# Kernel tuning notes

Hardware: AMD Instinct MI355X
Metric: run time of the kernel (lower is better)

Reference implementation:

```python
import jax, jax.numpy as jnp
import numpy as np

B, L, D, H = 32, 1024, 512, 512
ODE_STEPS = 6
DT = 1.0

def _unif(key, shape, fan_in):
    bound = 1.0 / np.sqrt(fan_in)
    return jax.random.uniform(key, shape, jnp.float32, -bound, bound)

def setup_inputs() -> dict:
    key = jax.random.key(0)
    ks = jax.random.split(key, 9)
    return {
        "x": jax.random.normal(ks[0], (B, L, D), jnp.float32),
        "log_tau": jnp.zeros((H,), jnp.float32),
        "W_in": _unif(ks[1], (H, D), D),
        "b_in": _unif(ks[2], (H,), D),
        "W_rec": _unif(ks[3], (H, H), H),
        "W_gate": _unif(ks[4], (H, D + H), D + H),
        "b_gate": _unif(ks[5], (H,), D + H),
        "W_out": _unif(ks[6], (H, H), H),
        "b_out": _unif(ks[7], (H,), H),
    }

def reference(x, log_tau, W_in, b_in, W_rec, W_gate, b_gate, W_out, b_out):
    Bx, Lx, Dx = x.shape
    Hx = log_tau.shape[0]
    tau = jnp.exp(log_tau)                      # (H,)
    sub_dt = DT / ODE_STEPS
    # Split gate weight: cat([x, h]) @ W_gate.T == x @ Wg_x.T + h @ Wg_h.T
    Wg_x, Wg_h = W_gate[:, :Dx], W_gate[:, Dx:]
    # Precompute input-dependent drives for the whole sequence (time-parallel GEMMs)
    drive = jnp.einsum('bld,hd->blh', x, W_in) + b_in      # W_in(x), (B,L,H)
    gate_x = jnp.einsum('bld,hd->blh', x, Wg_x) + b_gate   # input part of gate pre-act

    def step(h, inp):
        d, gx = inp  # (B,H) each
        for _ in range(ODE_STEPS):  # small fixed unroll of ODE sub-steps
            rec = h @ W_rec.T
            gate = jax.nn.sigmoid(gx + h @ Wg_h.T)
            f = -h + gate * jnp.tanh(d + rec)
            h = h + (sub_dt / tau) * f
        return h, h

    h0 = jnp.zeros((Bx, Hx), x.dtype)
    h_last, fwd = jax.lax.scan(step, h0, (drive.transpose(1, 0, 2), gate_x.transpose(1, 0, 2)))
    fwd = fwd.transpose(1, 0, 2)                 # (B,L,H)
    output = fwd @ W_out.T + b_out               # output_proj; dropout is identity (p=0)
    return output, h_last
```

## Files before the change

### kernel.cpp

```cpp
#include <hip/hip_runtime.h>

typedef unsigned short u16;
typedef unsigned int   u32;
typedef unsigned long long u64;

#define LTC_B 32
#define LTC_L 1024
#define LTC_D 512
#define LTC_H 512
#define NG 8
#define NP 16
#define NBG 4

typedef _Float16 f16x8  __attribute__((ext_vector_type(8)));
typedef _Float16 f16x2t __attribute__((ext_vector_type(2)));
typedef float    f32x4  __attribute__((ext_vector_type(4)));

static __device__ __forceinline__ u32 packh(float a, float b) {
    f16x2t p; p[0] = (_Float16)a; p[1] = (_Float16)b;
    return __builtin_bit_cast(u32, p);
}
static __device__ __forceinline__ float unplo(u32 w) {
    return (float)__builtin_bit_cast(f16x2t, w)[0];
}
static __device__ __forceinline__ float unphi(u32 w) {
    return (float)__builtin_bit_cast(f16x2t, w)[1];
}
static __device__ __forceinline__ float sigm(float x) {
    return 1.f / (1.f + __expf(-x));
}
static __device__ __forceinline__ float tanh_f(float x) {
    float e = __expf(2.f * x);
    return 1.f - 2.f / (e + 1.f);
}
static __device__ __forceinline__ f16x8 cvt8(const float* p) {
    const float4 a = *(const float4*)p;
    const float4 b = *(const float4*)(p + 4);
    f16x8 r;
    r[0] = (_Float16)a.x; r[1] = (_Float16)a.y; r[2] = (_Float16)a.z; r[3] = (_Float16)a.w;
    r[4] = (_Float16)b.x; r[5] = (_Float16)b.y; r[6] = (_Float16)b.z; r[7] = (_Float16)b.w;
    return r;
}
static __device__ __forceinline__ bool stamp4(u64 a, u64 b, u64 c, u64 d, u32 k) {
    return ((u32)(a >> 32) == k) & ((u32)(b >> 32) == k) &
           ((u32)(c >> 32) == k) & ((u32)(d >> 32) == k);
}

__global__ __launch_bounds__(256) void gemm_a32_c16(
    const float* __restrict__ A, const float* __restrict__ W, int ldb,
    const float* __restrict__ bias, u16* __restrict__ C)
{
    const int wave = threadIdx.x >> 6;
    const int lane = threadIdx.x & 63;
    const int tile = blockIdx.x * 4 + wave;
    const int nt = tile & 7;
    const int mt = tile >> 3;
    const int r16 = lane & 15;
    const int kq  = (lane >> 4) * 8;

    const float* ap = A + (size_t)(mt * 64 + r16) * LTC_D + kq;
    const float* wp = W + (size_t)(nt * 64 + r16) * ldb + kq;

    f32x4 acc[4][4];
    #pragma unroll
    for (int i = 0; i < 4; ++i)
        #pragma unroll
        for (int jj = 0; jj < 4; ++jj) acc[i][jj] = (f32x4){0.f, 0.f, 0.f, 0.f};

    for (int ks = 0; ks < 16; ++ks) {
        f16x8 af[4], bf[4];
        #pragma unroll
        for (int t = 0; t < 4; ++t) {
            af[t] = cvt8(ap + (size_t)t * 16 * LTC_D + ks * 32);
            bf[t] = cvt8(wp + (size_t)t * 16 * ldb  + ks * 32);
        }
        #pragma unroll
        for (int mi = 0; mi < 4; ++mi)
            #pragma unroll
            for (int ni = 0; ni < 4; ++ni)
                acc[mi][ni] = __builtin_amdgcn_mfma_f32_16x16x32_f16(
                    af[mi], bf[ni], acc[mi][ni], 0, 0, 0);
    }
    const int row = (lane >> 4) * 4;
    const int col = lane & 15;
    #pragma unroll
    for (int ni = 0; ni < 4; ++ni) {
        const int n = nt * 64 + ni * 16 + col;
        const float bv = bias[n];
        #pragma unroll
        for (int mi = 0; mi < 4; ++mi)
            #pragma unroll
            for (int r = 0; r < 4; ++r) {
                _Float16 h = (_Float16)(acc[mi][ni][r] + bv);
                C[(size_t)(mt * 64 + mi * 16 + row + r) * LTC_H + n] =
                    __builtin_bit_cast(u16, h);
            }
    }
}

__global__ __launch_bounds__(256) void gemm_a16_c32(
    const u16* __restrict__ A, const float* __restrict__ W,
    const float* __restrict__ bias, float* __restrict__ C)
{
    const int wave = threadIdx.x >> 6;
    const int lane = threadIdx.x & 63;
    const int tile = blockIdx.x * 4 + wave;
    const int nt = tile & 7;
    const int mt = tile >> 3;
    const int r16 = lane & 15;
    const int kq  = (lane >> 4) * 8;

    const _Float16* ap = (const _Float16*)A + (size_t)(mt * 64 + r16) * LTC_D + kq;
    const float*    wp = W + (size_t)(nt * 64 + r16) * LTC_H + kq;

    f32x4 acc[4][4];
    #pragma unroll
    for (int i = 0; i < 4; ++i)
        #pragma unroll
        for (int jj = 0; jj < 4; ++jj) acc[i][jj] = (f32x4){0.f, 0.f, 0.f, 0.f};

    for (int ks = 0; ks < 16; ++ks) {
        f16x8 af[4], bf[4];
        #pragma unroll
        for (int t = 0; t < 4; ++t) {
            af[t] = *(const f16x8*)(ap + (size_t)t * 16 * LTC_D + ks * 32);
            bf[t] = cvt8(wp + (size_t)t * 16 * LTC_H + ks * 32);
        }
        #pragma unroll
        for (int mi = 0; mi < 4; ++mi)
            #pragma unroll
            for (int ni = 0; ni < 4; ++ni)
                acc[mi][ni] = __builtin_amdgcn_mfma_f32_16x16x32_f16(
                    af[mi], bf[ni], acc[mi][ni], 0, 0, 0);
    }
    const int row = (lane >> 4) * 4;
    const int col = lane & 15;
    #pragma unroll
    for (int ni = 0; ni < 4; ++ni) {
        const int n = nt * 64 + ni * 16 + col;
        const float bv = bias[n];
        #pragma unroll
        for (int mi = 0; mi < 4; ++mi)
            #pragma unroll
            for (int r = 0; r < 4; ++r)
                C[(size_t)(mt * 64 + mi * 16 + row + r) * LTC_H + n] =
                    acc[mi][ni][r] + bv;
    }
}

__global__ __launch_bounds__(256) void ltc_scan(
    u32* __restrict__ drive,
    const u32* __restrict__ gatex,
    const float* __restrict__ W_rec,
    const float* __restrict__ W_gate,
    const float* __restrict__ log_tau,
    u64* __restrict__ hbuf,
    float* __restrict__ hlast)
{
    const int g   = blockIdx.x & 7;
    const int p   = blockIdx.x >> 3;
    const int tid = threadIdx.x;
    const int lane = tid & 63;
    const int wv   = tid >> 6;

    __shared__ u32 hTu[16][260];
    __shared__ float red[64][17];

    const int nl = wv * 16 + (lane & 15);
    const int kq = (lane >> 4) * 8;
    const float* wrow = (nl < 32)
        ? (W_rec  + (size_t)(32 * p + nl) * LTC_H)
        : (W_gate + (size_t)(32 * p + nl - 32) * (LTC_D + LTC_H) + LTC_D);
    f16x8 Wf[16];
    #pragma unroll
    for (int ks = 0; ks < 16; ++ks) Wf[ks] = cvt8(wrow + ks * 32 + kq);

    for (int i = tid; i < 16 * 260; i += 256) (&hTu[0][0])[i] = 0;
    __syncthreads();

    const int ub = tid >> 4;
    const int jp = tid & 15;
    const int j0 = 32 * p + 2 * jp;
    const int gb = g * NBG + ub;
    float h0 = 0.f, h1 = 0.f, stau0 = 0.f, stau1 = 0.f;
    size_t dwofs = 0;
    if (tid < 64) {
        stau0 = (1.f / 6.f) * __expf(-log_tau[j0]);
        stau1 = (1.f / 6.f) * __expf(-log_tau[j0 + 1]);
        dwofs = (size_t)gb * LTC_L * 256 + 16 * p + jp;
    }

    const _Float16* hrow = (const _Float16*)&hTu[lane & 15][0];
    u32 kp1 = 0;
    int budget = 1 << 22;
    const bool own = ((tid >> 4) == p);

    u32 dw = 0, gw = 0;
    if (tid < 64) { dw = drive[dwofs]; gw = gatex[dwofs]; }

    for (int l = 0; l < LTC_L; ++l) {
        const float d0 = unplo(dw), d1 = unphi(dw);
        const float gx0 = unplo(gw), gx1 = unphi(gw);
        u32 dn = 0, gn = 0;
        if (tid < 64 && l + 1 < LTC_L) {
            dn = drive[dwofs + (size_t)(l + 1) * 256];
            gn = gatex[dwofs + (size_t)(l + 1) * 256];
        }
        #pragma unroll 1
        for (int s = 0; s < 6; ++s) {
            f32x4 acc0 = (f32x4){0.f, 0.f, 0.f, 0.f}, acc1 = acc0;
            #pragma unroll
            for (int ks = 0; ks < 16; ks += 2) {
                const f16x8 a0 = *(const f16x8*)(hrow + ks * 32 + kq);
                const f16x8 a1 = *(const f16x8*)(hrow + (ks + 1) * 32 + kq);
                acc0 = __builtin_amdgcn_mfma_f32_16x16x32_f16(a0, Wf[ks],     acc0, 0, 0, 0);
                acc1 = __builtin_amdgcn_mfma_f32_16x16x32_f16(a1, Wf[ks + 1], acc1, 0, 0, 0);
            }
            {
                const int n  = wv * 16 + (lane & 15);
                const int rb = (lane >> 4) * 4;
                #pragma unroll
                for (int r = 0; r < 4; ++r) red[n][rb + r] = acc0[r] + acc1[r];
            }
            __syncthreads();
            ++kp1;
            const size_t pbase = (size_t)((kp1 & 1u) * NG + g) * (NBG * 256);
            if (tid < 64) {
                const float rec0 = red[2 * jp][ub],     gh0 = red[32 + 2 * jp][ub];
                const float rec1 = red[2 * jp + 1][ub], gh1 = red[32 + 2 * jp + 1][ub];
                h0 += stau0 * (sigm(gx0 + gh0) * tanh_f(d0 + rec0) - h0);
                h1 += stau1 * (sigm(gx1 + gh1) * tanh_f(d1 + rec1) - h1);
                const u32 pr = packh(h0, h1);
                hTu[ub][16 * p + jp] = pr;
                const u64 v = ((u64)kp1 << 32) | (u64)pr;
                __hip_atomic_store(hbuf + pbase + (size_t)ub * 256 + 16 * p + jp,
                                   v, __ATOMIC_RELAXED, __HIP_MEMORY_SCOPE_AGENT);
            }
            if (!own) {
                const u64* sb = hbuf + pbase + tid;
                u64 a0, a1, a2, a3;
                bool ok;
                do {
                    a0 = __hip_atomic_load(sb,       __ATOMIC_RELAXED,
                                           __HIP_MEMORY_SCOPE_AGENT);
                    a1 = __hip_atomic_load(sb + 256, __ATOMIC_RELAXED,
                                           __HIP_MEMORY_SCOPE_AGENT);
                    a2 = __hip_atomic_load(sb + 512, __ATOMIC_RELAXED,
                                           __HIP_MEMORY_SCOPE_AGENT);
                    a3 = __hip_atomic_load(sb + 768, __ATOMIC_RELAXED,
                                           __HIP_MEMORY_SCOPE_AGENT);
                    ok = stamp4(a0, a1, a2, a3, kp1);
                } while (!ok && --budget > 0);
                hTu[0][tid] = (u32)a0; hTu[1][tid] = (u32)a1;
                hTu[2][tid] = (u32)a2; hTu[3][tid] = (u32)a3;
            }
            __syncthreads();
        }
        if (tid < 64) drive[dwofs + (size_t)l * 256] = packh(h0, h1);
        dw = dn; gw = gn;
    }
    if (tid < 64) {
        hlast[(size_t)gb * LTC_H + j0]     = h0;
        hlast[(size_t)gb * LTC_H + j0 + 1] = h1;
    }
}

extern "C" void kernel_launch(void* const* d_in, const int* in_sizes, int n_in,
                              void* d_out, int out_size, void* d_ws, size_t ws_size,
                              hipStream_t stream)
{
    const float* x       = (const float*)d_in[0];
    const float* log_tau = (const float*)d_in[1];
    const float* W_in    = (const float*)d_in[2];
    const float* b_in    = (const float*)d_in[3];
    const float* W_rec   = (const float*)d_in[4];
    const float* W_gate  = (const float*)d_in[5];
    const float* b_gate  = (const float*)d_in[6];
    const float* W_out   = (const float*)d_in[7];
    const float* b_out   = (const float*)d_in[8];

    float* out   = (float*)d_out;
    float* hlast = out + (size_t)LTC_B * LTC_L * LTC_H;

    u32* ws    = (u32*)d_ws;
    u32* drive = ws;
    u32* gatex = ws + 8388608;
    u64* hbuf  = (u64*)(ws + 16777216);

    const int blocks = (LTC_B * LTC_L / 64) * (LTC_H / 64) / 4;

    gemm_a32_c16<<<blocks, 256, 0, stream>>>(x, W_in, LTC_D, b_in, (u16*)drive);
    gemm_a32_c16<<<blocks, 256, 0, stream>>>(x, W_gate, LTC_D + LTC_H, b_gate, (u16*)gatex);
    ltc_scan<<<NG * NP, 256, 0, stream>>>(drive, gatex, W_rec, W_gate, log_tau,
                                          hbuf, hlast);
    gemm_a16_c32<<<blocks, 256, 0, stream>>>((const u16*)drive, W_out, b_out, out);
}
```

Measured before the change: 10.88 ms.

## Add dedicated update wavefront to scan kernel, separating pointwise update from MFMA waves

The scan kernel now launches 320 threads: four waves hold the recurrent weights and do the MFMA matvec and the cross-block spin-wait, while a fifth wave does the pointwise ODE update and publishes h. The intent is to take the update work and the prefetch loads off the MFMA waves, which eases register pressure and splits the roles. It also zeroes hbuf at the start of the kernel and restructures the poll loop so the first loads are issued before the stamp check. In exchange, the extra wave uses more registers and adds one more sync participant to every substep.

```diff
diff --git a/kernel.cpp b/kernel.cpp
--- a/kernel.cpp
+++ b/kernel.cpp
@@ -148,7 +148,7 @@
     }
 }
 
-__global__ __launch_bounds__(256) void ltc_scan(
+__global__ __launch_bounds__(320) void ltc_scan(
     u32* __restrict__ drive,
     const u32* __restrict__ gatex,
     const float* __restrict__ W_rec,
@@ -166,100 +166,120 @@
     __shared__ u32 hTu[16][260];
     __shared__ float red[64][17];
 
-    const int nl = wv * 16 + (lane & 15);
     const int kq = (lane >> 4) * 8;
-    const float* wrow = (nl < 32)
-        ? (W_rec  + (size_t)(32 * p + nl) * LTC_H)
-        : (W_gate + (size_t)(32 * p + nl - 32) * (LTC_D + LTC_H) + LTC_D);
+
     f16x8 Wf[16];
-    #pragma unroll
-    for (int ks = 0; ks < 16; ++ks) Wf[ks] = cvt8(wrow + ks * 32 + kq);
-
-    for (int i = tid; i < 16 * 260; i += 256) (&hTu[0][0])[i] = 0;
-    __syncthreads();
-
-    const int ub = tid >> 4;
-    const int jp = tid & 15;
+    if (wv < 4) {
+        const int nl = wv * 16 + (lane & 15);
+        const float* wrow = (nl < 32)
+            ? (W_rec  + (size_t)(32 * p + nl) * LTC_H)
+            : (W_gate + (size_t)(32 * p + nl - 32) * (LTC_D + LTC_H) + LTC_D);
+        #pragma unroll
+        for (int ks = 0; ks < 16; ++ks) Wf[ks] = cvt8(wrow + ks * 32 + kq);
+    }
+
+    for (int i = tid; i < 16 * 260; i += 320) (&hTu[0][0])[i] = 0;
+
+    const int ut = tid - 256;
+    const bool isupd = (ut >= 0);
+    const int ub = ut >> 4;
+    const int jp = ut & 15;
     const int j0 = 32 * p + 2 * jp;
     const int gb = g * NBG + ub;
     float h0 = 0.f, h1 = 0.f, stau0 = 0.f, stau1 = 0.f;
     size_t dwofs = 0;
-    if (tid < 64) {
+    if (isupd) {
         stau0 = (1.f / 6.f) * __expf(-log_tau[j0]);
         stau1 = (1.f / 6.f) * __expf(-log_tau[j0 + 1]);
         dwofs = (size_t)gb * LTC_L * 256 + 16 * p + jp;
-    }
+        __hip_atomic_store(hbuf + (size_t)g * (NBG * 256) + (size_t)ub * 256
+                               + 16 * p + jp,
+                           0ull, __ATOMIC_RELAXED, __HIP_MEMORY_SCOPE_AGENT);
+    }
+    __syncthreads();
 
     const _Float16* hrow = (const _Float16*)&hTu[lane & 15][0];
+    const int redn = wv * 16 + (lane & 15);
+    const int redb = (lane >> 4) * 4;
     u32 kp1 = 0;
     int budget = 1 << 22;
-    const bool own = ((tid >> 4) == p);
+    const bool pskip = ((tid >> 4) == p);
 
     u32 dw = 0, gw = 0;
-    if (tid < 64) { dw = drive[dwofs]; gw = gatex[dwofs]; }
+    if (isupd) { dw = drive[dwofs]; gw = gatex[dwofs]; }
 
     for (int l = 0; l < LTC_L; ++l) {
         const float d0 = unplo(dw), d1 = unphi(dw);
         const float gx0 = unplo(gw), gx1 = unphi(gw);
         u32 dn = 0, gn = 0;
-        if (tid < 64 && l + 1 < LTC_L) {
+        if (isupd && l + 1 < LTC_L) {
             dn = drive[dwofs + (size_t)(l + 1) * 256];
             gn = gatex[dwofs + (size_t)(l + 1) * 256];
         }
         #pragma unroll 1
         for (int s = 0; s < 6; ++s) {
-            f32x4 acc0 = (f32x4){0.f, 0.f, 0.f, 0.f}, acc1 = acc0;
-            #pragma unroll
-            for (int ks = 0; ks < 16; ks += 2) {
-                const f16x8 a0 = *(const f16x8*)(hrow + ks * 32 + kq);
-                const f16x8 a1 = *(const f16x8*)(hrow + (ks + 1) * 32 + kq);
-                acc0 = __builtin_amdgcn_mfma_f32_16x16x32_f16(a0, Wf[ks],     acc0, 0, 0, 0);
-                acc1 = __builtin_amdgcn_mfma_f32_16x16x32_f16(a1, Wf[ks + 1], acc1, 0, 0, 0);
-            }
-            {
-                const int n  = wv * 16 + (lane & 15);
-                const int rb = (lane >> 4) * 4;
+            const u32 knew = kp1 + 1;
+            const size_t pbNew = (size_t)((knew & 1u) * NG + g) * (NBG * 256);
+
+            if (wv < 4) {
+                f32x4 acc0 = (f32x4){0.f, 0.f, 0.f, 0.f}, acc1 = acc0;
                 #pragma unroll
-                for (int r = 0; r < 4; ++r) red[n][rb + r] = acc0[r] + acc1[r];
+                for (int ks = 0; ks < 16; ks += 2) {
+                    const f16x8 a0 = *(const f16x8*)(hrow + ks * 32 + kq);
+                    const f16x8 a1 = *(const f16x8*)(hrow + (ks + 1) * 32 + kq);
+                    acc0 = __builtin_amdgcn_mfma_f32_16x16x32_f16(a0, Wf[ks],     acc0, 0, 0, 0);
+                    acc1 = __builtin_amdgcn_mfma_f32_16x16x32_f16(a1, Wf[ks + 1], acc1, 0, 0, 0);
+                }
+                #pragma unroll
+                for (int r = 0; r < 4; ++r) red[redn][redb + r] = acc0[r] + acc1[r];
             }
             __syncthreads();
-            ++kp1;
-            const size_t pbase = (size_t)((kp1 & 1u) * NG + g) * (NBG * 256);
-            if (tid < 64) {
+
+            if (isupd) {
                 const float rec0 = red[2 * jp][ub],     gh0 = red[32 + 2 * jp][ub];
                 const float rec1 = red[2 * jp + 1][ub], gh1 = red[32 + 2 * jp + 1][ub];
                 h0 += stau0 * (sigm(gx0 + gh0) * tanh_f(d0 + rec0) - h0);
                 h1 += stau1 * (sigm(gx1 + gh1) * tanh_f(d1 + rec1) - h1);
                 const u32 pr = packh(h0, h1);
+                __hip_atomic_store(hbuf + pbNew + (size_t)ub * 256 + 16 * p + jp,
+                                   ((u64)knew << 32) | (u64)pr,
+                                   __ATOMIC_RELAXED, __HIP_MEMORY_SCOPE_AGENT);
                 hTu[ub][16 * p + jp] = pr;
-                const u64 v = ((u64)kp1 << 32) | (u64)pr;
-                __hip_atomic_store(hbuf + pbase + (size_t)ub * 256 + 16 * p + jp,
-                                   v, __ATOMIC_RELAXED, __HIP_MEMORY_SCOPE_AGENT);
-            }
-            if (!own) {
-                const u64* sb = hbuf + pbase + tid;
-                u64 a0, a1, a2, a3;
-                bool ok;
-                do {
-                    a0 = __hip_atomic_load(sb,       __ATOMIC_RELAXED,
-                                           __HIP_MEMORY_SCOPE_AGENT);
-                    a1 = __hip_atomic_load(sb + 256, __ATOMIC_RELAXED,
-                                           __HIP_MEMORY_SCOPE_AGENT);
-                    a2 = __hip_atomic_load(sb + 512, __ATOMIC_RELAXED,
-                                           __HIP_MEMORY_SCOPE_AGENT);
-                    a3 = __hip_atomic_load(sb + 768, __ATOMIC_RELAXED,
-                                           __HIP_MEMORY_SCOPE_AGENT);
-                    ok = stamp4(a0, a1, a2, a3, kp1);
-                } while (!ok && --budget > 0);
-                hTu[0][tid] = (u32)a0; hTu[1][tid] = (u32)a1;
-                hTu[2][tid] = (u32)a2; hTu[3][tid] = (u32)a3;
             }
             __syncthreads();
+
+            if (wv < 4 && !pskip) {
+                const u64* b0 = hbuf + pbNew + tid;
+                u64 a0 = __hip_atomic_load(b0,       __ATOMIC_RELAXED,
+                                           __HIP_MEMORY_SCOPE_AGENT);
+                u64 a1 = __hip_atomic_load(b0 + 256, __ATOMIC_RELAXED,
+                                           __HIP_MEMORY_SCOPE_AGENT);
+                u64 a2 = __hip_atomic_load(b0 + 512, __ATOMIC_RELAXED,
+                                           __HIP_MEMORY_SCOPE_AGENT);
+                u64 a3 = __hip_atomic_load(b0 + 768, __ATOMIC_RELAXED,
+                                           __HIP_MEMORY_SCOPE_AGENT);
+                while (!stamp4(a0, a1, a2, a3, knew) && --budget > 0) {
+                    a0 = __hip_atomic_load(b0,       __ATOMIC_RELAXED,
+                                           __HIP_MEMORY_SCOPE_AGENT);
+                    a1 = __hip_atomic_load(b0 + 256, __ATOMIC_RELAXED,
+                                           __HIP_MEMORY_SCOPE_AGENT);
+                    a2 = __hip_atomic_load(b0 + 512, __ATOMIC_RELAXED,
+                                           __HIP_MEMORY_SCOPE_AGENT);
+                    a3 = __hip_atomic_load(b0 + 768, __ATOMIC_RELAXED,
+                                           __HIP_MEMORY_SCOPE_AGENT);
+                }
+                hTu[0][tid] = (u32)a0;
+                hTu[1][tid] = (u32)a1;
+                hTu[2][tid] = (u32)a2;
+                hTu[3][tid] = (u32)a3;
+            }
+            __syncthreads();
+            kp1 = knew;
         }
-        if (tid < 64) drive[dwofs + (size_t)l * 256] = packh(h0, h1);
+        if (isupd) drive[dwofs + (size_t)l * 256] = packh(h0, h1);
         dw = dn; gw = gn;
     }
-    if (tid < 64) {
+    if (isupd) {
         hlast[(size_t)gb * LTC_H + j0]     = h0;
         hlast[(size_t)gb * LTC_H + j0 + 1] = h1;
     }
@@ -291,7 +311,7 @@
 
     gemm_a32_c16<<<blocks, 256, 0, stream>>>(x, W_in, LTC_D, b_in, (u16*)drive);
     gemm_a32_c16<<<blocks, 256, 0, stream>>>(x, W_gate, LTC_D + LTC_H, b_gate, (u16*)gatex);
-    ltc_scan<<<NG * NP, 256, 0, stream>>>(drive, gatex, W_rec, W_gate, log_tau,
+    ltc_scan<<<NG * NP, 320, 0, stream>>>(drive, gatex, W_rec, W_gate, log_tau,
                                           hbuf, hlast);
     gemm_a16_c32<<<blocks, 256, 0, stream>>>((const u16*)drive, W_out, b_out, out);
 }
```

After: 10.61 ms. 2.5% less time.
